# Optimization experiments

Hardware: AMD Instinct MI355X
Metric: run time of the kernel (lower is better)

## Reference

```python
import jax, jax.numpy as jnp
import numpy as np

B, N, C, K, D = 32, 4096, 37, 100, 512   # images, rois, classes(incl bg), max dets/class, feat dim
C1 = C - 1
SCORE_TH, NMS_TH = 0.1, 0.4
BBOX_STDS = jnp.array([0.1, 0.1, 0.2, 0.2], jnp.float32)
HS, WS, SCALE = 960.0, 1280.0, 1.6  # scaled image height/width, resize scale


def setup_inputs() -> dict:
    key = jax.random.key(0)
    k1, k2, k3, k4 = jax.random.split(key, 4)
    u = jax.random.uniform(k1, (B, N, 4))
    x1 = u[..., 0] * (WS - 160.0)
    y1 = u[..., 1] * (HS - 160.0)
    w = u[..., 2] * 140.0 + 20.0
    h = u[..., 3] * 140.0 + 20.0
    boxes = jnp.stack([x1, y1, x1 + w, y1 + h], -1)          # [B,N,4] in scaled coords
    box_deltas = jax.random.normal(k2, (B, N, 4 * C)) * 0.5   # [B,N,4C]
    scores = jax.nn.softmax(jax.random.normal(k3, (B, N, C)) * 2.0, axis=-1)  # [B,N,C]
    roi_features = jax.random.normal(k4, (B, N, D))           # [B,N,D]
    im_info = jnp.tile(jnp.array([[HS, WS, SCALE]], jnp.float32), (B, 1))     # [B,3]
    return dict(boxes=boxes, box_deltas=box_deltas, scores=scores,
                roi_features=roi_features, im_info=im_info)


def _decode_clip(boxes, deltas, im_info):
    # bbox_transform_inv with normalize stds, then clip_boxes, then /scale.
    d = deltas.reshape(B, N, C, 4) * BBOX_STDS                # [B,N,C,4]
    w = boxes[..., 2] - boxes[..., 0] + 1.0
    h = boxes[..., 3] - boxes[..., 1] + 1.0
    cx = boxes[..., 0] + 0.5 * w
    cy = boxes[..., 1] + 0.5 * h
    pcx = d[..., 0] * w[..., None] + cx[..., None]
    pcy = d[..., 1] * h[..., None] + cy[..., None]
    pw = jnp.exp(d[..., 2]) * w[..., None]
    ph = jnp.exp(d[..., 3]) * h[..., None]
    hmax = im_info[:, 0][:, None, None] - 1.0
    wmax = im_info[:, 1][:, None, None] - 1.0
    x1 = jnp.clip(pcx - 0.5 * pw, 0.0, wmax)
    y1 = jnp.clip(pcy - 0.5 * ph, 0.0, hmax)
    x2 = jnp.clip(pcx + 0.5 * pw, 0.0, wmax)
    y2 = jnp.clip(pcy + 0.5 * ph, 0.0, hmax)
    pred = jnp.stack([x1, y1, x2, y2], -1)                    # [B,N,C,4]
    return pred / im_info[:, 2][:, None, None, None]


def _pairwise_iou(b):
    # b: [K,4] -> [K,K]
    area = (b[:, 2] - b[:, 0]) * (b[:, 3] - b[:, 1])
    lt = jnp.maximum(b[:, None, :2], b[None, :, :2])
    rb = jnp.minimum(b[:, None, 2:], b[None, :, 2:])
    wh = jnp.clip(rb - lt, 0.0)
    inter = wh[..., 0] * wh[..., 1]
    return inter / (area[:, None] + area[None, :] - inter + 1e-8)


def _nms_one_class(cls_boxes, cls_scores, feats):
    # cls_boxes [N,4], cls_scores [N], feats [N,D] -> det [K, 4+1+D]
    s = jnp.where(cls_scores > SCORE_TH, cls_scores, -1.0)
    vals, idx = jax.lax.top_k(s, K)                           # sorted desc == torch.sort(desc)
    b = cls_boxes[idx]                                        # [K,4]
    ious = _pairwise_iou(b)                                   # [K,K]
    valid = vals > SCORE_TH
    rng = jnp.arange(K)

    def body(i, keep):
        sup = (ious[i] > NMS_TH) & (rng > i) & keep[i]
        return keep & ~sup

    keep = jax.lax.fori_loop(0, K, body, valid)               # greedy NMS, fixed size
    det = jnp.concatenate([b, vals[:, None], feats[idx]], -1)  # [K,5+D]
    return jnp.where(keep[:, None], det, 0.0)


def reference(boxes, box_deltas, scores, roi_features, im_info):
    pred = _decode_clip(boxes, box_deltas, im_info)           # [B,N,C,4]
    cls_boxes = pred[:, :, 1:, :]                             # drop background, [B,N,C1,4]
    cls_scores = scores[:, :, 1:]                             # [B,N,C1]
    per_image = jax.vmap(_nms_one_class, in_axes=(1, 1, None))  # over class axis
    per_batch = jax.vmap(per_image, in_axes=(0, 0, 0))          # over image axis
    return per_batch(cls_boxes, cls_scores, roi_features)     # [B,C1,K,5+D]
```

## Files before the change

kernel.cpp:

```cpp
#include <hip/hip_runtime.h>
#include <cmath>

#define BB 32
#define NN 4096
#define NC 37
#define C1 36
#define KK 100
#define DD 512
#define SCORE_TH 0.1f
#define NMS_TH 0.4f
#define CAND_CAP 4096
#define NT 256
#define NROWS (BB * C1 * KK)

__global__ __launch_bounds__(NT) void select_kernel(
    const float* __restrict__ boxes,
    const float* __restrict__ deltas,
    const float* __restrict__ scores,
    const float* __restrict__ im_info,
    float* __restrict__ wbox,
    float* __restrict__ wval,
    int*   __restrict__ widx,
    int*   __restrict__ wkeep)
{
#pragma clang fp contract(off)
    __shared__ unsigned long long cand[CAND_CAP];
    __shared__ int cnt;
    __shared__ float sbox[KK][4];
    __shared__ float sarea[KK];
    __shared__ float sval[KK];
    __shared__ int   sidx[KK];
    __shared__ int   skeep[KK];

    const int bc  = blockIdx.x;
    const int b   = bc / C1;
    const int c   = bc % C1;
    const int tid = threadIdx.x;

    if (tid == 0) cnt = 0;
    __syncthreads();

    for (int n = tid; n < NN; n += NT) {
        float v = scores[(b * NN + n) * NC + (c + 1)];
        if (v > SCORE_TH) {
            int pos = atomicAdd(&cnt, 1);
            unsigned int vb = __float_as_uint(v);
            cand[pos] = ((unsigned long long)vb << 32) | (unsigned int)(0xFFFFFFFFu - (unsigned int)n);
        }
    }
    __syncthreads();
    const int M = cnt;

    int P = 128;
    while (P < M) P <<= 1;
    for (int i = M + tid; i < P; i += NT) cand[i] = 0ULL;
    __syncthreads();

    for (int k = 2; k <= P; k <<= 1) {
        for (int j = k >> 1; j > 0; j >>= 1) {
            for (int i = tid; i < P; i += NT) {
                int ixj = i ^ j;
                if (ixj > i) {
                    unsigned long long a  = cand[i];
                    unsigned long long bb = cand[ixj];
                    bool desc = ((i & k) == 0);
                    if (desc ? (a < bb) : (a > bb)) {
                        cand[i]   = bb;
                        cand[ixj] = a;
                    }
                }
            }
            __syncthreads();
        }
    }

    const int V = (M < KK) ? M : KK;

    if (tid < KK) {
        int k = tid;
        if (k < V) {
            unsigned long long key = cand[k];
            float v = __uint_as_float((unsigned int)(key >> 32));
            int   n = (int)(0xFFFFFFFFu - (unsigned int)(key & 0xFFFFFFFFull));
            sval[k] = v;
            sidx[k] = n;
            skeep[k] = 1;

            const float* bp = boxes + (b * NN + n) * 4;
            float bx1 = bp[0], by1 = bp[1], bx2 = bp[2], by2 = bp[3];
            const float* dp = deltas + ((b * NN + n) * NC + (c + 1)) * 4;
            float d0 = dp[0] * 0.1f;
            float d1 = dp[1] * 0.1f;
            float d2 = dp[2] * 0.2f;
            float d3 = dp[3] * 0.2f;

            float w  = bx2 - bx1 + 1.0f;
            float h  = by2 - by1 + 1.0f;
            float cx = bx1 + 0.5f * w;
            float cy = by1 + 0.5f * h;
            float pcx = d0 * w + cx;
            float pcy = d1 * h + cy;
            float pw  = (float)exp((double)d2) * w;
            float ph  = (float)exp((double)d3) * h;

            float hmax = im_info[b * 3 + 0] - 1.0f;
            float wmax = im_info[b * 3 + 1] - 1.0f;
            float sc   = im_info[b * 3 + 2];

            float x1p = fminf(fmaxf(pcx - 0.5f * pw, 0.0f), wmax);
            float y1p = fminf(fmaxf(pcy - 0.5f * ph, 0.0f), hmax);
            float x2p = fminf(fmaxf(pcx + 0.5f * pw, 0.0f), wmax);
            float y2p = fminf(fmaxf(pcy + 0.5f * ph, 0.0f), hmax);
            x1p = x1p / sc; y1p = y1p / sc; x2p = x2p / sc; y2p = y2p / sc;

            sbox[k][0] = x1p; sbox[k][1] = y1p; sbox[k][2] = x2p; sbox[k][3] = y2p;
            sarea[k] = (x2p - x1p) * (y2p - y1p);
        } else {
            sval[k] = 0.0f; sidx[k] = 0; skeep[k] = 0;
            sbox[k][0] = sbox[k][1] = sbox[k][2] = sbox[k][3] = 0.0f;
            sarea[k] = 0.0f;
        }
    }
    __syncthreads();

    for (int i = 0; i < V; ++i) {
        if (tid < KK && tid > i && skeep[i] && skeep[tid]) {
            float ax1 = sbox[i][0], ay1 = sbox[i][1], ax2 = sbox[i][2], ay2 = sbox[i][3];
            float qx1 = sbox[tid][0], qy1 = sbox[tid][1], qx2 = sbox[tid][2], qy2 = sbox[tid][3];
            float ltx = fmaxf(ax1, qx1);
            float lty = fmaxf(ay1, qy1);
            float rbx = fminf(ax2, qx2);
            float rby = fminf(ay2, qy2);
            float iw = fmaxf(rbx - ltx, 0.0f);
            float ih = fmaxf(rby - lty, 0.0f);
            float inter = iw * ih;
            float denom = sarea[i] + sarea[tid];
            denom = denom - inter;
            denom = denom + 1e-8f;
            float iou = inter / denom;
            if (iou > NMS_TH) skeep[tid] = 0;
        }
        __syncthreads();
    }

    if (tid < KK) {
        int r = bc * KK + tid;
        wkeep[r] = skeep[tid];
        widx[r]  = sidx[tid];
        wval[r]  = sval[tid];
        wbox[r * 4 + 0] = sbox[tid][0];
        wbox[r * 4 + 1] = sbox[tid][1];
        wbox[r * 4 + 2] = sbox[tid][2];
        wbox[r * 4 + 3] = sbox[tid][3];
    }
}

__global__ __launch_bounds__(128) void emit_kernel(
    const float* __restrict__ feats,
    const float* __restrict__ wbox,
    const float* __restrict__ wval,
    const int*   __restrict__ widx,
    const int*   __restrict__ wkeep,
    float* __restrict__ out)
{
    const int r   = blockIdx.x;
    const int tid = threadIdx.x;
    const long long obase = (long long)r * 517;

    if (wkeep[r]) {
        const int bc = r / KK;
        const int b  = bc / C1;
        const int n  = widx[r];
        const float* fp = feats + (long long)(b * NN + n) * DD;
        for (int j = tid; j < 517; j += 128) {
            float v;
            if (j < 4)       v = wbox[r * 4 + j];
            else if (j == 4) v = wval[r];
            else             v = fp[j - 5];
            out[obase + j] = v;
        }
    } else {
        for (int j = tid; j < 517; j += 128) out[obase + j] = 0.0f;
    }
}

extern "C" void kernel_launch(void* const* d_in, const int* in_sizes, int n_in,
                              void* d_out, int out_size, void* d_ws, size_t ws_size,
                              hipStream_t stream) {
    const float* boxes    = (const float*)d_in[0];
    const float* deltas   = (const float*)d_in[1];
    const float* scores   = (const float*)d_in[2];
    const float* feats    = (const float*)d_in[3];
    const float* im_info  = (const float*)d_in[4];
    float* out = (float*)d_out;

    char* ws = (char*)d_ws;
    float* wbox = (float*)ws;                         ws += (size_t)NROWS * 4 * sizeof(float);
    float* wval = (float*)ws;                         ws += (size_t)NROWS * sizeof(float);
    int*   widx = (int*)ws;                           ws += (size_t)NROWS * sizeof(int);
    int*   wkeep = (int*)ws;

    select_kernel<<<dim3(BB * C1), dim3(NT), 0, stream>>>(
        boxes, deltas, scores, im_info, wbox, wval, widx, wkeep);
    emit_kernel<<<dim3(NROWS), dim3(128), 0, stream>>>(
        feats, wbox, wval, widx, wkeep, out);
}
```

Baseline: 601.9 us.

## Fuse select and emit kernels, write detections directly with nontemporal stores

Merges the NMS selection kernel and the feature-gather emit kernel into one kernel, so each (image, class) block writes its 100 output rows straight from shared memory. This drops the workspace round-trip and one launch, and uses float4 feature loads with nontemporal stores. The cost is that output writing now runs on only 1152 blocks of 4 wavefronts each, rather than 115200 small blocks. That cuts the parallelism available to hide memory latency during the roughly 236 MB output write, and the write runs after the serial sort and NMS in each block.

```diff
diff --git a/kernel.cpp b/kernel.cpp
--- a/kernel.cpp
+++ b/kernel.cpp
@@ -11,17 +11,14 @@
 #define NMS_TH 0.4f
 #define CAND_CAP 4096
 #define NT 256
-#define NROWS (BB * C1 * KK)
 
-__global__ __launch_bounds__(NT) void select_kernel(
+__global__ __launch_bounds__(NT) void detect_kernel(
     const float* __restrict__ boxes,
     const float* __restrict__ deltas,
     const float* __restrict__ scores,
+    const float* __restrict__ feats,
     const float* __restrict__ im_info,
-    float* __restrict__ wbox,
-    float* __restrict__ wval,
-    int*   __restrict__ widx,
-    int*   __restrict__ wkeep)
+    float* __restrict__ out)
 {
 #pragma clang fp contract(off)
     __shared__ unsigned long long cand[CAND_CAP];
@@ -143,44 +140,40 @@
         __syncthreads();
     }
 
-    if (tid < KK) {
-        int r = bc * KK + tid;
-        wkeep[r] = skeep[tid];
-        widx[r]  = sidx[tid];
-        wval[r]  = sval[tid];
-        wbox[r * 4 + 0] = sbox[tid][0];
-        wbox[r * 4 + 1] = sbox[tid][1];
-        wbox[r * 4 + 2] = sbox[tid][2];
-        wbox[r * 4 + 3] = sbox[tid][3];
-    }
-}
-
-__global__ __launch_bounds__(128) void emit_kernel(
-    const float* __restrict__ feats,
-    const float* __restrict__ wbox,
-    const float* __restrict__ wval,
-    const int*   __restrict__ widx,
-    const int*   __restrict__ wkeep,
-    float* __restrict__ out)
-{
-    const int r   = blockIdx.x;
-    const int tid = threadIdx.x;
-    const long long obase = (long long)r * 517;
-
-    if (wkeep[r]) {
-        const int bc = r / KK;
-        const int b  = bc / C1;
-        const int n  = widx[r];
-        const float* fp = feats + (long long)(b * NN + n) * DD;
-        for (int j = tid; j < 517; j += 128) {
-            float v;
-            if (j < 4)       v = wbox[r * 4 + j];
-            else if (j == 4) v = wval[r];
-            else             v = fp[j - 5];
-            out[obase + j] = v;
+    const int wv = tid >> 6;
+    const int ln = tid & 63;
+    const long long obase0 = (long long)bc * KK * 517;
+    for (int k = wv; k < KK; k += (NT / 64)) {
+        float* op = out + obase0 + (long long)k * 517;
+        if (skeep[k]) {
+            if (ln == 0) {
+                __builtin_nontemporal_store(sbox[k][0], op + 0);
+                __builtin_nontemporal_store(sbox[k][1], op + 1);
+                __builtin_nontemporal_store(sbox[k][2], op + 2);
+                __builtin_nontemporal_store(sbox[k][3], op + 3);
+                __builtin_nontemporal_store(sval[k],    op + 4);
+            }
+            const float4* f4 = (const float4*)(feats + (long long)(b * NN + sidx[k]) * DD);
+            float4 v0 = f4[ln];
+            float4 v1 = f4[ln + 64];
+            float* o5 = op + 5;
+            const int j0 = ln * 4;
+            __builtin_nontemporal_store(v0.x, o5 + j0 + 0);
+            __builtin_nontemporal_store(v0.y, o5 + j0 + 1);
+            __builtin_nontemporal_store(v0.z, o5 + j0 + 2);
+            __builtin_nontemporal_store(v0.w, o5 + j0 + 3);
+            const int j1 = (ln + 64) * 4;
+            __builtin_nontemporal_store(v1.x, o5 + j1 + 0);
+            __builtin_nontemporal_store(v1.y, o5 + j1 + 1);
+            __builtin_nontemporal_store(v1.z, o5 + j1 + 2);
+            __builtin_nontemporal_store(v1.w, o5 + j1 + 3);
+        } else {
+            #pragma unroll
+            for (int t = 0; t < 8; ++t)
+                __builtin_nontemporal_store(0.0f, op + t * 64 + ln);
+            if (ln < 5)
+                __builtin_nontemporal_store(0.0f, op + 512 + ln);
         }
-    } else {
-        for (int j = tid; j < 517; j += 128) out[obase + j] = 0.0f;
     }
 }
 
@@ -194,14 +187,6 @@
     const float* im_info  = (const float*)d_in[4];
     float* out = (float*)d_out;
 
-    char* ws = (char*)d_ws;
-    float* wbox = (float*)ws;                         ws += (size_t)NROWS * 4 * sizeof(float);
-    float* wval = (float*)ws;                         ws += (size_t)NROWS * sizeof(float);
-    int*   widx = (int*)ws;                           ws += (size_t)NROWS * sizeof(int);
-    int*   wkeep = (int*)ws;
-
-    select_kernel<<<dim3(BB * C1), dim3(NT), 0, stream>>>(
-        boxes, deltas, scores, im_info, wbox, wval, widx, wkeep);
-    emit_kernel<<<dim3(NROWS), dim3(128), 0, stream>>>(
-        feats, wbox, wval, widx, wkeep, out);
+    detect_kernel<<<dim3(BB * C1), dim3(NT), 0, stream>>>(
+        boxes, deltas, scores, feats, im_info, out);
 }
```

New measurement: 594.8 us. No clear change (-1.2%).
